# Kernel tuning notes

Hardware: AMD Instinct MI355X
Metric: run time of the kernel (lower is better)

Reference implementation:

```python
import jax, jax.numpy as jnp
import numpy as np
import math

HEAD = 4

def _neighbors3x3(t):
    # t: [b, g, d, h, w] -> [b, g, d, 9, h, w], zero-padded 3x3 neighborhoods
    b, g, d, h, w = t.shape
    tp = jnp.pad(t, ((0, 0), (0, 0), (0, 0), (1, 1), (1, 1)))
    # torch.nn.Unfold(kernel_size=3) ordering: kernel positions row-major (dy, dx)
    patches = [tp[:, :, :, dy:dy + h, dx:dx + w] for dy in range(3) for dx in range(3)]
    return jnp.stack(patches, axis=3)


def setup_inputs() -> dict:
    key = jax.random.key(0)
    k1, k2 = jax.random.split(key)
    x = jax.random.normal(k1, (8, 128, 96, 96), dtype=jnp.float32)
    # 1x1 conv weight, no bias: [out=3*out_features, in=in_features]
    W_trans = jax.random.normal(k2, (384, 128), dtype=jnp.float32) * 0.05
    return {"x": x, "W_trans": W_trans}


def reference(x, W_trans):
    b, cin, h, w = x.shape
    # 1x1 conv == channel GEMM
    t = jnp.einsum('bchw,oc->bohw', x, W_trans)  # [b, 3*C, h, w]
    q, k, v = jnp.split(t, 3, axis=1)            # each [b, C, h, w]
    C = q.shape[1]
    d = C // HEAD
    q = q.reshape(b, HEAD, d, h, w)
    k = k.reshape(b, HEAD, d, h, w)
    v = v.reshape(b, HEAD, d, h, w)
    kn = _neighbors3x3(k)  # [b, g, d, 9, h, w]
    vn = _neighbors3x3(v)  # [b, g, d, 9, h, w]
    # att[b,g,n,h,w] = <q[b,g,:,h,w], kn[b,g,:,n,h,w]> / sqrt(d)
    att = jnp.einsum('bgdhw,bgdnhw->bgnhw', q, kn) / math.sqrt(d)
    att = jax.nn.softmax(att, axis=2)
    # dropout p=0.4 is identity in eval mode
    out = jnp.einsum('bgnhw,bgdnhw->bgdhw', att, vn)  # [b, g, d, h, w]
    return out.reshape(b, C, h, w)
```

## Files before the change

### kernel.cpp

```cpp
#include <hip/hip_runtime.h>

#define NB     8
#define CIN    128
#define HEADS  4
#define DHEAD  32
#define HDIM   96
#define WDIM   96
#define HW     9216
#define TP     32

typedef __bf16 bf16x8 __attribute__((ext_vector_type(8)));
typedef float  f32x4  __attribute__((ext_vector_type(4)));

__device__ __forceinline__ unsigned f2bf(float f) {
  unsigned u = __float_as_uint(f);
  return (u + 0x7fffu + ((u >> 16) & 1u)) >> 16;
}
__device__ __forceinline__ unsigned pack2(float a, float b) {
  return f2bf(a) | (f2bf(b) << 16);
}
__device__ __forceinline__ float bflo(unsigned u) { return __uint_as_float(u << 16); }
__device__ __forceinline__ float bfhi(unsigned u) { return __uint_as_float(u & 0xffff0000u); }

__global__ __launch_bounds__(256) void wpack_kernel(const float* __restrict__ W,
                                                    uint4* __restrict__ Wf) {
  const int u = blockIdx.x * 256 + threadIdx.x;
  const int lane = u & 63, kb = (u >> 6) & 3, ot = u >> 8;
  const int o = ot * 16 + (lane & 15);
  const int c0 = kb * 32 + (lane >> 4) * 8;
  const float4* w = (const float4*)(W + (size_t)o * CIN + c0);
  float4 w0 = w[0], w1 = w[1];
  uint4 r;
  r.x = pack2(w0.x, w0.y); r.y = pack2(w0.z, w0.w);
  r.z = pack2(w1.x, w1.y); r.w = pack2(w1.z, w1.w);
  Wf[u] = r;
}

__global__ __launch_bounds__(256) void qkv_kernel(const float* __restrict__ x,
                                                  const uint4* __restrict__ Wf,
                                                  unsigned short* __restrict__ qkvb) {
  __shared__ uint4 xs[8 * 64];
  const int b  = blockIdx.y;
  const int p0 = blockIdx.x * TP;
  const int t  = threadIdx.x;

#pragma unroll
  for (int i = 0; i < 2; ++i) {
    const int slot = i * 256 + t;
    const int px = slot & 31, oct = slot >> 5;
    const int c0 = oct * 8;
    const float* xb = x + ((size_t)b * CIN + c0) * HW + p0 + px;
    float f[8];
#pragma unroll
    for (int j = 0; j < 8; ++j) f[j] = xb[(size_t)j * HW];
    uint4 r;
    r.x = pack2(f[0], f[1]); r.y = pack2(f[2], f[3]);
    r.z = pack2(f[4], f[5]); r.w = pack2(f[6], f[7]);
    const int pt = px >> 4, n = px & 15, kb = oct >> 2, q = oct & 3;
    xs[(pt * 4 + kb) * 64 + q * 16 + n] = r;
  }
  __syncthreads();

  const int wv = t >> 6, lane = t & 63;
  const int colp = lane & 15, quad = lane >> 4;
#pragma unroll
  for (int it = 0; it < 6; ++it) {
    const int ot = wv * 6 + it;
    bf16x8 afrag[4];
#pragma unroll
    for (int kb = 0; kb < 4; ++kb) {
      uint4 tmp = Wf[(ot * 4 + kb) * 64 + lane];
      afrag[kb] = *(bf16x8*)&tmp;
    }
    const int o0 = ot * 16 + quad * 4;
    const int which = o0 >> 7, g = (o0 & 127) >> 5, d0 = o0 & 31;
    unsigned short* dst = qkvb
        + (((size_t)(which * NB + b) * HEADS + g) * HW) * DHEAD + d0;
#pragma unroll
    for (int pt = 0; pt < 2; ++pt) {
      f32x4 acc = {0.f, 0.f, 0.f, 0.f};
#pragma unroll
      for (int kb = 0; kb < 4; ++kb) {
        bf16x8 bfrag = *(bf16x8*)&xs[(pt * 4 + kb) * 64 + lane];
        acc = __builtin_amdgcn_mfma_f32_16x16x32_bf16(afrag[kb], bfrag, acc, 0, 0, 0);
      }
      const int pp = p0 + pt * 16 + colp;
      uint2 st;
      st.x = pack2(acc[0], acc[1]);
      st.y = pack2(acc[2], acc[3]);
      *(uint2*)(dst + (size_t)pp * DHEAD) = st;
    }
  }
}

__global__ __launch_bounds__(256) void attn_kernel(const unsigned short* __restrict__ qkvb,
                                                   float* __restrict__ out) {
  const int tx = threadIdx.x;
  const int wq = tx & 31, dh = tx >> 5;
  const int w  = blockIdx.x * 32 + wq;
  const int h  = blockIdx.y * 4 + threadIdx.y;
  const int bg = blockIdx.z;
  const int b  = bg >> 2, g = bg & 3;

  const size_t plane = (size_t)HW * DHEAD;
  const unsigned short* Qb = qkvb + (size_t)bg * plane;
  const unsigned short* Kb = qkvb + (size_t)(32 + bg) * plane;
  const unsigned short* Vb = qkvb + (size_t)(64 + bg) * plane;
  const int p = h * WDIM + w;

  float q[16];
  {
    const uint4* qp = (const uint4*)(Qb + (size_t)p * DHEAD + dh * 16);
    uint4 u0 = qp[0], u1 = qp[1];
    q[0] = bflo(u0.x); q[1] = bfhi(u0.x); q[2] = bflo(u0.y); q[3] = bfhi(u0.y);
    q[4] = bflo(u0.z); q[5] = bfhi(u0.z); q[6] = bflo(u0.w); q[7] = bfhi(u0.w);
    q[8]  = bflo(u1.x); q[9]  = bfhi(u1.x); q[10] = bflo(u1.y); q[11] = bfhi(u1.y);
    q[12] = bflo(u1.z); q[13] = bfhi(u1.z); q[14] = bflo(u1.w); q[15] = bfhi(u1.w);
  }

  float att[9];
#pragma unroll
  for (int dy = -1; dy <= 1; ++dy) {
    const int hh = h + dy;
    const int hc = min(max(hh, 0), HDIM - 1);
    const bool rowOK = (unsigned)hh < (unsigned)HDIM;
#pragma unroll
    for (int dx = -1; dx <= 1; ++dx) {
      const int nn = (dy + 1) * 3 + (dx + 1);
      const int ww = w + dx;
      const int wc = min(max(ww, 0), WDIM - 1);
      const bool ok = rowOK && ((unsigned)ww < (unsigned)WDIM);
      const int pn = hc * WDIM + wc;
      const uint4* kp = (const uint4*)(Kb + (size_t)pn * DHEAD + dh * 16);
      uint4 k0 = kp[0], k1 = kp[1];
      float dot = 0.f;
      dot = fmaf(q[0], bflo(k0.x), dot);  dot = fmaf(q[1], bfhi(k0.x), dot);
      dot = fmaf(q[2], bflo(k0.y), dot);  dot = fmaf(q[3], bfhi(k0.y), dot);
      dot = fmaf(q[4], bflo(k0.z), dot);  dot = fmaf(q[5], bfhi(k0.z), dot);
      dot = fmaf(q[6], bflo(k0.w), dot);  dot = fmaf(q[7], bfhi(k0.w), dot);
      dot = fmaf(q[8],  bflo(k1.x), dot); dot = fmaf(q[9],  bfhi(k1.x), dot);
      dot = fmaf(q[10], bflo(k1.y), dot); dot = fmaf(q[11], bfhi(k1.y), dot);
      dot = fmaf(q[12], bflo(k1.z), dot); dot = fmaf(q[13], bfhi(k1.z), dot);
      dot = fmaf(q[14], bflo(k1.w), dot); dot = fmaf(q[15], bfhi(k1.w), dot);
      dot += __shfl_xor(dot, 32);
      att[nn] = ok ? dot * 0.17677669529663687f : 0.f;
    }
  }

  float m = att[0];
#pragma unroll
  for (int nn = 1; nn < 9; ++nn) m = fmaxf(m, att[nn]);
  float s = 0.f;
#pragma unroll
  for (int nn = 0; nn < 9; ++nn) { att[nn] = __expf(att[nn] - m); s += att[nn]; }
  const float inv = 1.0f / s;

  float acc[16];
#pragma unroll
  for (int i = 0; i < 16; ++i) acc[i] = 0.f;
#pragma unroll
  for (int dy = -1; dy <= 1; ++dy) {
    const int hh = h + dy;
    const int hc = min(max(hh, 0), HDIM - 1);
    const bool rowOK = (unsigned)hh < (unsigned)HDIM;
#pragma unroll
    for (int dx = -1; dx <= 1; ++dx) {
      const int nn = (dy + 1) * 3 + (dx + 1);
      const int ww = w + dx;
      const int wc = min(max(ww, 0), WDIM - 1);
      const bool ok = rowOK && ((unsigned)ww < (unsigned)WDIM);
      const int pn = hc * WDIM + wc;
      const float wn = ok ? att[nn] * inv : 0.f;
      const uint4* vp = (const uint4*)(Vb + (size_t)pn * DHEAD + dh * 16);
      uint4 v0 = vp[0], v1 = vp[1];
      acc[0] = fmaf(wn, bflo(v0.x), acc[0]);  acc[1] = fmaf(wn, bfhi(v0.x), acc[1]);
      acc[2] = fmaf(wn, bflo(v0.y), acc[2]);  acc[3] = fmaf(wn, bfhi(v0.y), acc[3]);
      acc[4] = fmaf(wn, bflo(v0.z), acc[4]);  acc[5] = fmaf(wn, bfhi(v0.z), acc[5]);
      acc[6] = fmaf(wn, bflo(v0.w), acc[6]);  acc[7] = fmaf(wn, bfhi(v0.w), acc[7]);
      acc[8]  = fmaf(wn, bflo(v1.x), acc[8]);  acc[9]  = fmaf(wn, bfhi(v1.x), acc[9]);
      acc[10] = fmaf(wn, bflo(v1.y), acc[10]); acc[11] = fmaf(wn, bfhi(v1.y), acc[11]);
      acc[12] = fmaf(wn, bflo(v1.z), acc[12]); acc[13] = fmaf(wn, bfhi(v1.z), acc[13]);
      acc[14] = fmaf(wn, bflo(v1.w), acc[14]); acc[15] = fmaf(wn, bfhi(v1.w), acc[15]);
    }
  }

  float* ob = out + ((size_t)b * CIN + (size_t)g * DHEAD + dh * 16) * HW + p;
#pragma unroll
  for (int i = 0; i < 16; ++i) ob[(size_t)i * HW] = acc[i];
}

extern "C" void kernel_launch(void* const* d_in, const int* in_sizes, int n_in,
                              void* d_out, int out_size, void* d_ws, size_t ws_size,
                              hipStream_t stream) {
  (void)in_sizes; (void)n_in; (void)out_size; (void)ws_size;
  const float* x = (const float*)d_in[0];
  const float* W = (const float*)d_in[1];
  float* out = (float*)d_out;

  const size_t qkv_ushorts = (size_t)3 * NB * HEADS * HW * DHEAD;
  unsigned short* qkvb = (unsigned short*)d_ws;
  uint4* Wf = (uint4*)((char*)d_ws + qkv_ushorts * 2);

  wpack_kernel<<<24, 256, 0, stream>>>(W, Wf);
  qkv_kernel<<<dim3(HW / TP, NB), 256, 0, stream>>>(x, Wf, qkvb);
  attn_kernel<<<dim3(WDIM / 32, HDIM / 4, NB * HEADS), dim3(64, 4, 1), 0, stream>>>(qkvb, out);
}
```

Baseline: 128.4 us.

## Fuse QKV projection and neighborhood attention into one tiled kernel with halo recompute

Replaces the separate QKV GEMM and attention kernels with one fused kernel. Each block loads a 4x16 pixel tile plus a one-pixel halo of x, computes Q/K/V for two heads with MFMA into shared memory, then runs the 3x3 attention from LDS. The aim is to drop the bf16 QKV round trip through global memory and a kernel launch. The cost is recomputing K/V on halo pixels (108 vs 64 pixels, padded to 112), heavier shared-memory use, and x being read twice because each batch is split into two head-pair blocks.

```diff
diff --git a/kernel.cpp b/kernel.cpp
--- a/kernel.cpp
+++ b/kernel.cpp
@@ -1,13 +1,18 @@
 #include <hip/hip_runtime.h>
 
-#define NB     8
-#define CIN    128
-#define HEADS  4
-#define DHEAD  32
-#define HDIM   96
-#define WDIM   96
-#define HW     9216
-#define TP     32
+#define NB    8
+#define CIN   128
+#define HDIM  96
+#define WDIM  96
+#define HW    9216
+#define TW    16
+#define TH    4
+#define HXW   18
+#define NHX   108
+#define NHXP  112
+#define NMT   7
+#define KV_REC 272
+#define Q_REC  144
 
 typedef __bf16 bf16x8 __attribute__((ext_vector_type(8)));
 typedef float  f32x4  __attribute__((ext_vector_type(4)));
@@ -36,157 +41,147 @@
   Wf[u] = r;
 }
 
-__global__ __launch_bounds__(256) void qkv_kernel(const float* __restrict__ x,
-                                                  const uint4* __restrict__ Wf,
-                                                  unsigned short* __restrict__ qkvb) {
-  __shared__ uint4 xs[8 * 64];
-  const int b  = blockIdx.y;
-  const int p0 = blockIdx.x * TP;
+__global__ __launch_bounds__(256, 2) void fused_kernel(
+    const float* __restrict__ x, const uint4* __restrict__ Wf,
+    float* __restrict__ out) {
+  __shared__ uint4 xs4[NMT * 4 * 64];
+  __shared__ uint4 kv4[NHXP * KV_REC / 16];
+  __shared__ uint4 q4[NHXP * Q_REC / 16];
+
   const int t  = threadIdx.x;
+  const int w0 = blockIdx.x * TW, h0 = blockIdx.y * TH;
+  const int b  = blockIdx.z >> 1, hp = blockIdx.z & 1;
 
 #pragma unroll
-  for (int i = 0; i < 2; ++i) {
-    const int slot = i * 256 + t;
-    const int px = slot & 31, oct = slot >> 5;
-    const int c0 = oct * 8;
-    const float* xb = x + ((size_t)b * CIN + c0) * HW + p0 + px;
+  for (int i = 0; i < 7; ++i) {
+    const int id  = i * 256 + t;
+    const int oct = id / NHXP;
+    const int hx  = id - oct * NHXP;
+    const int r   = hx / HXW;
+    const int ww  = hx - r * HXW;
+    const int h = h0 - 1 + r, w = w0 - 1 + ww;
+    const bool valid = (hx < NHX) && ((unsigned)h < HDIM) && ((unsigned)w < WDIM);
     float f[8];
+    if (valid) {
+      const float* xb = x + ((size_t)(b * CIN + oct * 8)) * HW + h * WDIM + w;
 #pragma unroll
-    for (int j = 0; j < 8; ++j) f[j] = xb[(size_t)j * HW];
-    uint4 r;
-    r.x = pack2(f[0], f[1]); r.y = pack2(f[2], f[3]);
-    r.z = pack2(f[4], f[5]); r.w = pack2(f[6], f[7]);
-    const int pt = px >> 4, n = px & 15, kb = oct >> 2, q = oct & 3;
-    xs[(pt * 4 + kb) * 64 + q * 16 + n] = r;
+      for (int jv = 0; jv < 8; ++jv) f[jv] = xb[(size_t)jv * HW];
+    } else {
+#pragma unroll
+      for (int jv = 0; jv < 8; ++jv) f[jv] = 0.f;
+    }
+    uint4 rv;
+    rv.x = pack2(f[0], f[1]); rv.y = pack2(f[2], f[3]);
+    rv.z = pack2(f[4], f[5]); rv.w = pack2(f[6], f[7]);
+    xs4[((hx >> 4) * 4 + (oct >> 2)) * 64 + (oct & 3) * 16 + (hx & 15)] = rv;
   }
   __syncthreads();
 
-  const int wv = t >> 6, lane = t & 63;
-  const int colp = lane & 15, quad = lane >> 4;
+  {
+    const int lane = t & 63, wv = t >> 6;
+    const int colp = lane & 15, quad = lane >> 4;
+    uint4 bfr[NMT][4];
 #pragma unroll
-  for (int it = 0; it < 6; ++it) {
-    const int ot = wv * 6 + it;
-    bf16x8 afrag[4];
+    for (int mt = 0; mt < NMT; ++mt)
 #pragma unroll
-    for (int kb = 0; kb < 4; ++kb) {
-      uint4 tmp = Wf[(ot * 4 + kb) * 64 + lane];
-      afrag[kb] = *(bf16x8*)&tmp;
-    }
-    const int o0 = ot * 16 + quad * 4;
-    const int which = o0 >> 7, g = (o0 & 127) >> 5, d0 = o0 & 31;
-    unsigned short* dst = qkvb
-        + (((size_t)(which * NB + b) * HEADS + g) * HW) * DHEAD + d0;
+      for (int kb = 0; kb < 4; ++kb)
+        bfr[mt][kb] = xs4[(mt * 4 + kb) * 64 + lane];
+
 #pragma unroll
-    for (int pt = 0; pt < 2; ++pt) {
-      f32x4 acc = {0.f, 0.f, 0.f, 0.f};
+    for (int jj = 0; jj < 3; ++jj) {
+      const int j = wv * 3 + jj;
+      const int which = j >> 2, jo = j & 3;
+      const int ot = which * 8 + hp * 4 + jo;
+      uint4 af[4];
 #pragma unroll
-      for (int kb = 0; kb < 4; ++kb) {
-        bf16x8 bfrag = *(bf16x8*)&xs[(pt * 4 + kb) * 64 + lane];
-        acc = __builtin_amdgcn_mfma_f32_16x16x32_bf16(afrag[kb], bfrag, acc, 0, 0, 0);
+      for (int kb = 0; kb < 4; ++kb) af[kb] = Wf[(ot * 4 + kb) * 64 + lane];
+      const int lc = jo * 16 + quad * 4;
+      char* base; int rec;
+      if (which == 0) { base = (char*)q4 + lc * 2; rec = Q_REC; }
+      else { base = (char*)kv4 + (which - 1) * 128 + lc * 2; rec = KV_REC; }
+#pragma unroll
+      for (int mt = 0; mt < NMT; ++mt) {
+        f32x4 acc = {0.f, 0.f, 0.f, 0.f};
+#pragma unroll
+        for (int kb = 0; kb < 4; ++kb)
+          acc = __builtin_amdgcn_mfma_f32_16x16x32_bf16(
+              *(bf16x8*)&af[kb], *(bf16x8*)&bfr[mt][kb], acc, 0, 0, 0);
+        uint2 st;
+        st.x = pack2(acc[0], acc[1]);
+        st.y = pack2(acc[2], acc[3]);
+        *(uint2*)(base + (mt * 16 + colp) * rec) = st;
       }
-      const int pp = p0 + pt * 16 + colp;
-      uint2 st;
-      st.x = pack2(acc[0], acc[1]);
-      st.y = pack2(acc[2], acc[3]);
-      *(uint2*)(dst + (size_t)pp * DHEAD) = st;
     }
   }
-}
+  __syncthreads();
 
-__global__ __launch_bounds__(256) void attn_kernel(const unsigned short* __restrict__ qkvb,
-                                                   float* __restrict__ out) {
-  const int tx = threadIdx.x;
-  const int wq = tx & 31, dh = tx >> 5;
-  const int w  = blockIdx.x * 32 + wq;
-  const int h  = blockIdx.y * 4 + threadIdx.y;
-  const int bg = blockIdx.z;
-  const int b  = bg >> 2, g = bg & 3;
+  {
+    const int px = t >> 2, g2 = (t >> 1) & 1, dh = t & 1;
+    const int pr = px >> 4, pw = px & 15;
+    const int hx0 = (pr + 1) * HXW + pw + 1;
+    const int hoff = g2 * 64 + dh * 32;
 
-  const size_t plane = (size_t)HW * DHEAD;
-  const unsigned short* Qb = qkvb + (size_t)bg * plane;
-  const unsigned short* Kb = qkvb + (size_t)(32 + bg) * plane;
-  const unsigned short* Vb = qkvb + (size_t)(64 + bg) * plane;
-  const int p = h * WDIM + w;
+    float q[16];
+    {
+      const uint4* qp = (const uint4*)((const char*)q4 + hx0 * Q_REC + hoff);
+      uint4 u0 = qp[0], u1 = qp[1];
+      q[0]=bflo(u0.x);  q[1]=bfhi(u0.x);  q[2]=bflo(u0.y);  q[3]=bfhi(u0.y);
+      q[4]=bflo(u0.z);  q[5]=bfhi(u0.z);  q[6]=bflo(u0.w);  q[7]=bfhi(u0.w);
+      q[8]=bflo(u1.x);  q[9]=bfhi(u1.x);  q[10]=bflo(u1.y); q[11]=bfhi(u1.y);
+      q[12]=bflo(u1.z); q[13]=bfhi(u1.z); q[14]=bflo(u1.w); q[15]=bfhi(u1.w);
+    }
 
-  float q[16];
-  {
-    const uint4* qp = (const uint4*)(Qb + (size_t)p * DHEAD + dh * 16);
-    uint4 u0 = qp[0], u1 = qp[1];
-    q[0] = bflo(u0.x); q[1] = bfhi(u0.x); q[2] = bflo(u0.y); q[3] = bfhi(u0.y);
-    q[4] = bflo(u0.z); q[5] = bfhi(u0.z); q[6] = bflo(u0.w); q[7] = bfhi(u0.w);
-    q[8]  = bflo(u1.x); q[9]  = bfhi(u1.x); q[10] = bflo(u1.y); q[11] = bfhi(u1.y);
-    q[12] = bflo(u1.z); q[13] = bfhi(u1.z); q[14] = bflo(u1.w); q[15] = bfhi(u1.w);
-  }
-
-  float att[9];
+    float att[9];
 #pragma unroll
-  for (int dy = -1; dy <= 1; ++dy) {
-    const int hh = h + dy;
-    const int hc = min(max(hh, 0), HDIM - 1);
-    const bool rowOK = (unsigned)hh < (unsigned)HDIM;
-#pragma unroll
-    for (int dx = -1; dx <= 1; ++dx) {
-      const int nn = (dy + 1) * 3 + (dx + 1);
-      const int ww = w + dx;
-      const int wc = min(max(ww, 0), WDIM - 1);
-      const bool ok = rowOK && ((unsigned)ww < (unsigned)WDIM);
-      const int pn = hc * WDIM + wc;
-      const uint4* kp = (const uint4*)(Kb + (size_t)pn * DHEAD + dh * 16);
+    for (int nn = 0; nn < 9; ++nn) {
+      const int hxn = hx0 + (nn / 3 - 1) * HXW + (nn % 3 - 1);
+      const uint4* kp = (const uint4*)((const char*)kv4 + hxn * KV_REC + hoff);
       uint4 k0 = kp[0], k1 = kp[1];
       float dot = 0.f;
-      dot = fmaf(q[0], bflo(k0.x), dot);  dot = fmaf(q[1], bfhi(k0.x), dot);
-      dot = fmaf(q[2], bflo(k0.y), dot);  dot = fmaf(q[3], bfhi(k0.y), dot);
-      dot = fmaf(q[4], bflo(k0.z), dot);  dot = fmaf(q[5], bfhi(k0.z), dot);
-      dot = fmaf(q[6], bflo(k0.w), dot);  dot = fmaf(q[7], bfhi(k0.w), dot);
+      dot = fmaf(q[0],  bflo(k0.x), dot); dot = fmaf(q[1],  bfhi(k0.x), dot);
+      dot = fmaf(q[2],  bflo(k0.y), dot); dot = fmaf(q[3],  bfhi(k0.y), dot);
+      dot = fmaf(q[4],  bflo(k0.z), dot); dot = fmaf(q[5],  bfhi(k0.z), dot);
+      dot = fmaf(q[6],  bflo(k0.w), dot); dot = fmaf(q[7],  bfhi(k0.w), dot);
       dot = fmaf(q[8],  bflo(k1.x), dot); dot = fmaf(q[9],  bfhi(k1.x), dot);
       dot = fmaf(q[10], bflo(k1.y), dot); dot = fmaf(q[11], bfhi(k1.y), dot);
       dot = fmaf(q[12], bflo(k1.z), dot); dot = fmaf(q[13], bfhi(k1.z), dot);
       dot = fmaf(q[14], bflo(k1.w), dot); dot = fmaf(q[15], bfhi(k1.w), dot);
-      dot += __shfl_xor(dot, 32);
-      att[nn] = ok ? dot * 0.17677669529663687f : 0.f;
+      dot += __shfl_xor(dot, 1);
+      att[nn] = dot * 0.17677669529663687f;
     }
-  }
 
-  float m = att[0];
+    float m = att[0];
 #pragma unroll
-  for (int nn = 1; nn < 9; ++nn) m = fmaxf(m, att[nn]);
-  float s = 0.f;
+    for (int nn = 1; nn < 9; ++nn) m = fmaxf(m, att[nn]);
+    float s = 0.f;
 #pragma unroll
-  for (int nn = 0; nn < 9; ++nn) { att[nn] = __expf(att[nn] - m); s += att[nn]; }
-  const float inv = 1.0f / s;
+    for (int nn = 0; nn < 9; ++nn) { att[nn] = __expf(att[nn] - m); s += att[nn]; }
+    const float inv = 1.0f / s;
 
-  float acc[16];
+    float acc[16];
 #pragma unroll
-  for (int i = 0; i < 16; ++i) acc[i] = 0.f;
+    for (int i = 0; i < 16; ++i) acc[i] = 0.f;
 #pragma unroll
-  for (int dy = -1; dy <= 1; ++dy) {
-    const int hh = h + dy;
-    const int hc = min(max(hh, 0), HDIM - 1);
-    const bool rowOK = (unsigned)hh < (unsigned)HDIM;
-#pragma unroll
-    for (int dx = -1; dx <= 1; ++dx) {
-      const int nn = (dy + 1) * 3 + (dx + 1);
-      const int ww = w + dx;
-      const int wc = min(max(ww, 0), WDIM - 1);
-      const bool ok = rowOK && ((unsigned)ww < (unsigned)WDIM);
-      const int pn = hc * WDIM + wc;
-      const float wn = ok ? att[nn] * inv : 0.f;
-      const uint4* vp = (const uint4*)(Vb + (size_t)pn * DHEAD + dh * 16);
+    for (int nn = 0; nn < 9; ++nn) {
+      const int hxn = hx0 + (nn / 3 - 1) * HXW + (nn % 3 - 1);
+      const uint4* vp = (const uint4*)((const char*)kv4 + hxn * KV_REC + 128 + hoff);
       uint4 v0 = vp[0], v1 = vp[1];
-      acc[0] = fmaf(wn, bflo(v0.x), acc[0]);  acc[1] = fmaf(wn, bfhi(v0.x), acc[1]);
-      acc[2] = fmaf(wn, bflo(v0.y), acc[2]);  acc[3] = fmaf(wn, bfhi(v0.y), acc[3]);
-      acc[4] = fmaf(wn, bflo(v0.z), acc[4]);  acc[5] = fmaf(wn, bfhi(v0.z), acc[5]);
-      acc[6] = fmaf(wn, bflo(v0.w), acc[6]);  acc[7] = fmaf(wn, bfhi(v0.w), acc[7]);
+      const float wn = att[nn] * inv;
+      acc[0]  = fmaf(wn, bflo(v0.x), acc[0]);  acc[1]  = fmaf(wn, bfhi(v0.x), acc[1]);
+      acc[2]  = fmaf(wn, bflo(v0.y), acc[2]);  acc[3]  = fmaf(wn, bfhi(v0.y), acc[3]);
+      acc[4]  = fmaf(wn, bflo(v0.z), acc[4]);  acc[5]  = fmaf(wn, bfhi(v0.z), acc[5]);
+      acc[6]  = fmaf(wn, bflo(v0.w), acc[6]);  acc[7]  = fmaf(wn, bfhi(v0.w), acc[7]);
       acc[8]  = fmaf(wn, bflo(v1.x), acc[8]);  acc[9]  = fmaf(wn, bfhi(v1.x), acc[9]);
       acc[10] = fmaf(wn, bflo(v1.y), acc[10]); acc[11] = fmaf(wn, bfhi(v1.y), acc[11]);
       acc[12] = fmaf(wn, bflo(v1.z), acc[12]); acc[13] = fmaf(wn, bfhi(v1.z), acc[13]);
       acc[14] = fmaf(wn, bflo(v1.w), acc[14]); acc[15] = fmaf(wn, bfhi(v1.w), acc[15]);
     }
+
+    float* ob = out + ((size_t)(b * CIN + hp * 64 + g2 * 32 + dh * 16)) * HW
+                + (h0 + pr) * WDIM + w0 + pw;
+#pragma unroll
+    for (int i = 0; i < 16; ++i) ob[(size_t)i * HW] = acc[i];
   }
-
-  float* ob = out + ((size_t)b * CIN + (size_t)g * DHEAD + dh * 16) * HW + p;
-#pragma unroll
-  for (int i = 0; i < 16; ++i) ob[(size_t)i * HW] = acc[i];
 }
 
 extern "C" void kernel_launch(void* const* d_in, const int* in_sizes, int n_in,
@@ -196,12 +191,8 @@
   const float* x = (const float*)d_in[0];
   const float* W = (const float*)d_in[1];
   float* out = (float*)d_out;
-
-  const size_t qkv_ushorts = (size_t)3 * NB * HEADS * HW * DHEAD;
-  unsigned short* qkvb = (unsigned short*)d_ws;
-  uint4* Wf = (uint4*)((char*)d_ws + qkv_ushorts * 2);
+  uint4* Wf = (uint4*)d_ws;
 
   wpack_kernel<<<24, 256, 0, stream>>>(W, Wf);
-  qkv_kernel<<<dim3(HW / TP, NB), 256, 0, stream>>>(x, Wf, qkvb);
-  attn_kernel<<<dim3(WDIM / 32, HDIM / 4, NB * HEADS), dim3(64, 4, 1), 0, stream>>>(qkvb, out);
+  fused_kernel<<<dim3(WDIM / TW, HDIM / TH, NB * 2), 256, 0, stream>>>(x, Wf, out);
 }
```

Result: no change. 130.5 us (+1.7%).
